# Kernel tuning notes

Hardware: AMD Instinct MI355X
Metric: run time of the kernel (lower is better)

The kernel has to match this reference:

```python
import jax, jax.numpy as jnp
import numpy as np

B, H, W = 16, 64, 64
C_IN, C_OUT, W_DIM = 256, 128, 128


def modulated_conv2d(x, kernel, style):
    """StyleGAN2 modulated+demodulated conv, vmapped over batch.
    x: [B,H,W,C_in], kernel: [kH,kW,C_in,C_out], style: [B,C_in]."""
    kH = kernel.shape[0]
    pad = kH // 2

    def conv_single(x_i, s_i):
        kern = kernel * s_i[None, None, :, None]
        denom = jnp.sqrt(jnp.sum(kern ** 2, axis=(0, 1, 2), keepdims=True) + 1e-08)
        kern = kern / denom
        return jax.lax.conv_general_dilated(
            x_i[None], kern, window_strides=(1, 1),
            padding=((pad, pad), (pad, pad)),
            dimension_numbers=('NHWC', 'HWIO', 'NHWC'))[0]

    return jax.vmap(conv_single)(x, style)


def pixel_shuffle(x, scale=2):
    b, h, w, c = x.shape
    s = scale
    c_out = c // (s * s)
    x = x.reshape(b, h, w, s, s, c_out)
    x = x.transpose(0, 1, 3, 2, 4, 5)
    return x.reshape(b, h * s, w * s, c_out)


def setup_inputs() -> dict:
    key = jax.random.key(0)
    ks = jax.random.split(key, 12)
    dense_std = 1.0 / np.sqrt(W_DIM)  # lecun_normal-like for Dense
    return {
        'x': jax.random.normal(ks[0], (B, H, W, C_IN), jnp.float32),
        'w': jax.random.normal(ks[1], (B, W_DIM), jnp.float32),
        'affine1_w': jax.random.normal(ks[2], (W_DIM, C_IN), jnp.float32) * dense_std,
        'affine1_b': jnp.ones((C_IN,), jnp.float32),  # bias_init=ones
        'kernel1': jax.random.normal(ks[3], (3, 3, C_IN, C_IN), jnp.float32),
        'noise_scale1': jnp.full((1,), 0.1, jnp.float32),
        'bias1': jax.random.normal(ks[4], (C_IN,), jnp.float32) * 0.02,
        'affine2_w': jax.random.normal(ks[5], (W_DIM, C_IN), jnp.float32) * dense_std,
        'affine2_b': jnp.ones((C_IN,), jnp.float32),
        'kernel2': jax.random.normal(ks[6], (3, 3, C_IN, C_OUT * 4), jnp.float32),
        'noise_scale2': jnp.full((1,), 0.1, jnp.float32),
        'bias2': jax.random.normal(ks[7], (C_OUT * 4,), jnp.float32) * 0.02,
        'noise1': jax.random.normal(ks[8], (B, H, W, 1), jnp.float32),
        'noise2': jax.random.normal(ks[9], (B, H, W, 1), jnp.float32),
    }


def reference(x, w, affine1_w, affine1_b, kernel1, noise_scale1, bias1,
              affine2_w, affine2_b, kernel2, noise_scale2, bias2,
              noise1, noise2):
    # style affine 1 -> modulated conv (C_in -> C_in)
    s1 = w @ affine1_w + affine1_b                      # [B, C_in]
    h = modulated_conv2d(x, kernel1, s1)                # [B,H,W,C_in]
    h = h + noise1 * noise_scale1
    h = jax.nn.leaky_relu(h + bias1, negative_slope=0.2)
    # style affine 2 -> modulated conv (C_in -> 4*C_out)
    s2 = w @ affine2_w + affine2_b                      # [B, C_in]
    h = modulated_conv2d(h, kernel2, s2)                # [B,H,W,4*C_out]
    h = h + noise2 * noise_scale2
    h = jax.nn.leaky_relu(h + bias2, negative_slope=0.2)
    return pixel_shuffle(h, scale=2)                    # [B,2H,2W,C_out]
```

## Files before the change

kernel.cpp:

```cpp
#include <hip/hip_runtime.h>
#include <type_traits>


#define CIN 256

typedef _Float16 half4 __attribute__((ext_vector_type(4)));
typedef _Float16 half8 __attribute__((ext_vector_type(8)));
typedef float f32x4 __attribute__((ext_vector_type(4)));

__global__ __launch_bounds__(256) void style_kernel(
    const float* __restrict__ w, const float* __restrict__ a1w, const float* __restrict__ a1b,
    const float* __restrict__ a2w, const float* __restrict__ a2b,
    float* __restrict__ s1, float* __restrict__ s2)
{
  const int b = blockIdx.x, c = threadIdx.x;
  const float* wb = w + b * 128;
  float acc1 = 0.f, acc2 = 0.f;
  for (int k = 0; k < 128; ++k) {
    const float wv = wb[k];
    acc1 = fmaf(wv, a1w[k * 256 + c], acc1);
    acc2 = fmaf(wv, a2w[k * 256 + c], acc2);
  }
  s1[b * 256 + c] = acc1 + a1b[c];
  s2[b * 256 + c] = acc2 + a2b[c];
}

__global__ __launch_bounds__(256) void ksq_kernel(
    const float* __restrict__ kern, float* __restrict__ ksq, int n)
{
  const int i = blockIdx.x * 256 + threadIdx.x;
  if (i < n) {
    float acc = 0.f;
    for (int t = 0; t < 9; ++t) { const float v = kern[t * n + i]; acc = fmaf(v, v, acc); }
    ksq[i] = acc;
  }
}

__global__ __launch_bounds__(256) void demod_kernel(
    const float* __restrict__ s, const float* __restrict__ ksq,
    float* __restrict__ demod, int cout)
{
  const int b = blockIdx.y;
  const int o = blockIdx.x * 256 + threadIdx.x;
  const float* sb = s + b * 256;
  float acc = 1e-8f;
  for (int i = 0; i < 256; ++i) {
    const float sv = sb[i];
    acc = fmaf(sv * sv, ksq[i * cout + o], acc);
  }
  demod[b * cout + o] = 1.0f / sqrtf(acc);
}

__global__ __launch_bounds__(256) void kprep_kernel(
    const float* __restrict__ Kw, _Float16* __restrict__ Bt, int cout)
{
  __shared__ float T[64][68];
  const int tap = blockIdx.z;
  const int o0 = blockIdx.x * 64, c0 = blockIdx.y * 64;
  const int t = threadIdx.x;
  #pragma unroll
  for (int it = 0; it < 4; ++it) {
    const int c = (t >> 4) + it * 16;
    const int o = (t & 15) * 4;
    *(float4*)(&T[c][o]) = *(const float4*)(Kw + ((size_t)tap * CIN + c0 + c) * cout + o0 + o);
  }
  __syncthreads();
  #pragma unroll
  for (int it = 0; it < 4; ++it) {
    const int o = (t >> 4) + it * 16;
    const int c = (t & 15) * 4;
    half4 hv = {(_Float16)T[c][o], (_Float16)T[c + 1][o],
                (_Float16)T[c + 2][o], (_Float16)T[c + 3][o]};
    *(half4*)(&Bt[((size_t)tap * cout + o0 + o) * CIN + c0 + c]) = hv;
  }
}

template <int COUT, bool SHUFFLE, typename TIN, typename TOUT>
__global__ __launch_bounds__(256) void conv_mfma(
    const TIN* __restrict__ X,
    const float* __restrict__ S,
    const _Float16* __restrict__ Bt,
    const float* __restrict__ D,
    const float* __restrict__ NZ,
    const float* __restrict__ NSp,
    const float* __restrict__ BIAS,
    TOUT* __restrict__ OUT)
{
  __shared__ __align__(16) _Float16 As[66][72];
  __shared__ __align__(16) _Float16 Bs[3][64][72];
  __shared__ float Ss[256];

  const int t = threadIdx.x;
  const int row = blockIdx.x;
  const int b = row >> 6, y = row & 63;
  const int o0 = blockIdx.y * 64;

  Ss[t] = S[b * 256 + t];

  const int lane = t & 63, wid = t >> 6;
  const int wm = wid >> 1, wn = wid & 1;
  const int lrow = lane >> 4;
  const int lcol = lane & 15;

  f32x4 acc[2][2];
  #pragma unroll
  for (int m = 0; m < 2; ++m)
    #pragma unroll
    for (int n = 0; n < 2; ++n)
      acc[m][n] = (f32x4){0.f, 0.f, 0.f, 0.f};

  const TIN* Xb = X + (size_t)b * (64 * 64 * CIN);

  for (int dyi = 0; dyi < 3; ++dyi) {
    const int ys = y + dyi - 1;
    const bool vrow = ((unsigned)ys < 64u);
    const TIN* Xrow = Xb + (size_t)ys * (64 * CIN);

    for (int c0 = 0; c0 < CIN; c0 += 64) {
      __syncthreads();
      #pragma unroll
      for (int it = 0; it < 5; ++it) {
        const int r = (t >> 4) + it * 16;
        if (r < 66) {
          const int xs = r - 1;
          const int cq = (t & 15) * 4;
          half4 hv = {(_Float16)0, (_Float16)0, (_Float16)0, (_Float16)0};
          if (vrow && (unsigned)xs < 64u) {
            const float4 sv = *(const float4*)(Ss + c0 + cq);
            if constexpr (std::is_same_v<TIN, float>) {
              const float4 xv = *(const float4*)(Xrow + (size_t)xs * CIN + c0 + cq);
              hv[0] = (_Float16)(xv.x * sv.x);
              hv[1] = (_Float16)(xv.y * sv.y);
              hv[2] = (_Float16)(xv.z * sv.z);
              hv[3] = (_Float16)(xv.w * sv.w);
            } else {
              const half4 xv = *(const half4*)(Xrow + (size_t)xs * CIN + c0 + cq);
              hv[0] = (_Float16)((float)xv[0] * sv.x);
              hv[1] = (_Float16)((float)xv[1] * sv.y);
              hv[2] = (_Float16)((float)xv[2] * sv.z);
              hv[3] = (_Float16)((float)xv[3] * sv.w);
            }
          }
          *(half4*)(&As[r][cq]) = hv;
        }
      }
      #pragma unroll
      for (int dxi = 0; dxi < 3; ++dxi) {
        const int tap = dyi * 3 + dxi;
        const _Float16* Bsrc = Bt + ((size_t)tap * COUT + o0) * CIN + c0;
        #pragma unroll
        for (int it = 0; it < 2; ++it) {
          const int n = (t >> 3) + it * 32;
          const int hq = (t & 7) * 8;
          *(half8*)(&Bs[dxi][n][hq]) = *(const half8*)(Bsrc + (size_t)n * CIN + hq);
        }
      }
      __syncthreads();
      #pragma unroll
      for (int dxi = 0; dxi < 3; ++dxi) {
        const int abase = dxi + wm * 32 + lcol;
        #pragma unroll
        for (int ks = 0; ks < 2; ++ks) {
          const int ko = ks * 32 + lrow * 8;
          const half8 a0 = *(const half8*)(&As[abase][ko]);
          const half8 a1 = *(const half8*)(&As[abase + 16][ko]);
          const half8 b0 = *(const half8*)(&Bs[dxi][wn * 32 + lcol][ko]);
          const half8 b1 = *(const half8*)(&Bs[dxi][wn * 32 + 16 + lcol][ko]);
          acc[0][0] = __builtin_amdgcn_mfma_f32_16x16x32_f16(a0, b0, acc[0][0], 0, 0, 0);
          acc[0][1] = __builtin_amdgcn_mfma_f32_16x16x32_f16(a0, b1, acc[0][1], 0, 0, 0);
          acc[1][0] = __builtin_amdgcn_mfma_f32_16x16x32_f16(a1, b0, acc[1][0], 0, 0, 0);
          acc[1][1] = __builtin_amdgcn_mfma_f32_16x16x32_f16(a1, b1, acc[1][1], 0, 0, 0);
        }
      }
    }
  }

  const float ns = NSp[0];
  #pragma unroll
  for (int n = 0; n < 2; ++n) {
    const int o = o0 + wn * 32 + n * 16 + lcol;
    const float dmv = D[b * COUT + o];
    const float bv = BIAS[o];
    #pragma unroll
    for (int m = 0; m < 2; ++m) {
      #pragma unroll
      for (int r = 0; r < 4; ++r) {
        const int p = wm * 32 + m * 16 + lrow * 4 + r;
        const float nzv = NZ[(size_t)(b * 64 + y) * 64 + p] * ns;
        float v = fmaf(acc[m][n][r], dmv, nzv + bv);
        v = fmaxf(v, 0.2f * v);
        if (!SHUFFLE) {
          OUT[((size_t)(b * 64 + y) * 64 + p) * COUT + o] = (TOUT)v;
        } else {
          const int g = o >> 7, c = o & 127;
          const int sh = g >> 1, sw = g & 1;
          OUT[(((size_t)(b * 128) + 2 * y + sh) * 128 + (2 * p + sw)) * 128 + c] = (TOUT)v;
        }
      }
    }
  }
}

extern "C" void kernel_launch(void* const* d_in, const int* in_sizes, int n_in,
                              void* d_out, int out_size, void* d_ws, size_t ws_size,
                              hipStream_t stream)
{
  const float* x   = (const float*)d_in[0];
  const float* w   = (const float*)d_in[1];
  const float* a1w = (const float*)d_in[2];
  const float* a1b = (const float*)d_in[3];
  const float* k1  = (const float*)d_in[4];
  const float* ns1 = (const float*)d_in[5];
  const float* b1  = (const float*)d_in[6];
  const float* a2w = (const float*)d_in[7];
  const float* a2b = (const float*)d_in[8];
  const float* k2  = (const float*)d_in[9];
  const float* ns2 = (const float*)d_in[10];
  const float* b2  = (const float*)d_in[11];
  const float* nz1 = (const float*)d_in[12];
  const float* nz2 = (const float*)d_in[13];
  float* out = (float*)d_out;

  float* ws = (float*)d_ws;
  float* s1   = ws;
  float* s2   = ws + 4096;
  float* ksq1 = ws + 8192;
  float* ksq2 = ws + 73728;
  float* dm1  = ws + 204800;
  float* dm2  = ws + 208896;
  _Float16* Bt1 = (_Float16*)(ws + 217088);
  _Float16* Bt2 = Bt1 + 9 * 256 * 256;
  _Float16* h   = Bt2 + 9 * 512 * 256;

  style_kernel<<<16, 256, 0, stream>>>(w, a1w, a1b, a2w, a2b, s1, s2);
  ksq_kernel<<<65536 / 256, 256, 0, stream>>>(k1, ksq1, 65536);
  ksq_kernel<<<131072 / 256, 256, 0, stream>>>(k2, ksq2, 131072);
  demod_kernel<<<dim3(1, 16), 256, 0, stream>>>(s1, ksq1, dm1, 256);
  demod_kernel<<<dim3(2, 16), 256, 0, stream>>>(s2, ksq2, dm2, 512);
  kprep_kernel<<<dim3(4, 4, 9), 256, 0, stream>>>(k1, Bt1, 256);
  kprep_kernel<<<dim3(8, 4, 9), 256, 0, stream>>>(k2, Bt2, 512);

  conv_mfma<256, false, float, _Float16><<<dim3(1024, 4), 256, 0, stream>>>(
      x, s1, Bt1, dm1, nz1, ns1, b1, h);
  conv_mfma<512, true, _Float16, float><<<dim3(1024, 8), 256, 0, stream>>>(
      h, s2, Bt2, dm2, nz2, ns2, b2, out);
}
```

Measured before the change: 696.9 us.

## Widen conv tiles to 128 outputs, fold style2 into conv1 epilogue, swizzle blocks

Each workgroup now computes 128 output channels with 512 threads, so every staged input row is reused across twice as many outputs. The second conv's style modulation is folded into the first conv's epilogue, letting conv2 load fp16 activations directly with no per-element multiply. A linear block index is remapped so that consecutive blocks are spread across groups of eight, which is meant to improve cache locality. In exchange the B tile in LDS doubles in size, which raises shared-memory use and may reduce occupancy.

```diff
diff --git a/kernel.cpp b/kernel.cpp
--- a/kernel.cpp
+++ b/kernel.cpp
@@ -75,32 +75,37 @@
   }
 }
 
-template <int COUT, bool SHUFFLE, typename TIN, typename TOUT>
-__global__ __launch_bounds__(256) void conv_mfma(
+template <int COUT, bool AMOD, bool SHUFFLE, typename TIN, typename TOUT>
+__global__ __launch_bounds__(512) void conv_mfma(
     const TIN* __restrict__ X,
-    const float* __restrict__ S,
+    const float* __restrict__ Sg,
     const _Float16* __restrict__ Bt,
     const float* __restrict__ D,
     const float* __restrict__ NZ,
     const float* __restrict__ NSp,
     const float* __restrict__ BIAS,
+    const float* __restrict__ SMOD,
     TOUT* __restrict__ OUT)
 {
   __shared__ __align__(16) _Float16 As[66][72];
-  __shared__ __align__(16) _Float16 Bs[3][64][72];
-  __shared__ float Ss[256];
+  __shared__ __align__(16) _Float16 Bs[3][128][72];
 
   const int t = threadIdx.x;
-  const int row = blockIdx.x;
+  constexpr int nwg = (COUT / 128) * 1024;
+  constexpr int q = nwg >> 3;
+  const int lin = blockIdx.x;
+  const int wgid = (lin & 7) * q + (lin >> 3);
+  const int row = wgid & 1023, oc = wgid >> 10;
   const int b = row >> 6, y = row & 63;
-  const int o0 = blockIdx.y * 64;
-
-  Ss[t] = S[b * 256 + t];
+  const int o0 = oc * 128;
 
   const int lane = t & 63, wid = t >> 6;
-  const int wm = wid >> 1, wn = wid & 1;
+  const int wm = wid & 1, wn = wid >> 1;
   const int lrow = lane >> 4;
   const int lcol = lane & 15;
+
+  const int sr = t >> 3;
+  const int sco = (t & 7) * 8;
 
   f32x4 acc[2][2];
   #pragma unroll
@@ -109,50 +114,48 @@
     for (int n = 0; n < 2; ++n)
       acc[m][n] = (f32x4){0.f, 0.f, 0.f, 0.f};
 
-  const TIN* Xb = X + (size_t)b * (64 * 64 * CIN);
+  const TIN* Xb = X + (size_t)b * (64 * 64 * 256);
 
   for (int dyi = 0; dyi < 3; ++dyi) {
     const int ys = y + dyi - 1;
     const bool vrow = ((unsigned)ys < 64u);
-    const TIN* Xrow = Xb + (size_t)ys * (64 * CIN);
-
-    for (int c0 = 0; c0 < CIN; c0 += 64) {
+    const TIN* Xrow = Xb + (size_t)(vrow ? ys : 0) * (64 * 256);
+
+    for (int c0 = 0; c0 < 256; c0 += 64) {
       __syncthreads();
       #pragma unroll
-      for (int it = 0; it < 5; ++it) {
-        const int r = (t >> 4) + it * 16;
-        if (r < 66) {
+      for (int part = 0; part < 2; ++part) {
+        const int r = part ? 64 + (t >> 3) : sr;
+        if (part == 0 || t < 16) {
           const int xs = r - 1;
-          const int cq = (t & 15) * 4;
-          half4 hv = {(_Float16)0, (_Float16)0, (_Float16)0, (_Float16)0};
-          if (vrow && (unsigned)xs < 64u) {
-            const float4 sv = *(const float4*)(Ss + c0 + cq);
-            if constexpr (std::is_same_v<TIN, float>) {
-              const float4 xv = *(const float4*)(Xrow + (size_t)xs * CIN + c0 + cq);
-              hv[0] = (_Float16)(xv.x * sv.x);
-              hv[1] = (_Float16)(xv.y * sv.y);
-              hv[2] = (_Float16)(xv.z * sv.z);
-              hv[3] = (_Float16)(xv.w * sv.w);
+          const bool v = vrow && ((unsigned)xs < 64u);
+          half8 hv = {(_Float16)0, (_Float16)0, (_Float16)0, (_Float16)0,
+                      (_Float16)0, (_Float16)0, (_Float16)0, (_Float16)0};
+          if (v) {
+            if constexpr (AMOD) {
+              const float4 x0 = *(const float4*)(Xrow + (size_t)xs * 256 + c0 + sco);
+              const float4 x1 = *(const float4*)(Xrow + (size_t)xs * 256 + c0 + sco + 4);
+              const float4 s0 = *(const float4*)(Sg + b * 256 + c0 + sco);
+              const float4 s1v = *(const float4*)(Sg + b * 256 + c0 + sco + 4);
+              hv[0] = (_Float16)(x0.x * s0.x);  hv[1] = (_Float16)(x0.y * s0.y);
+              hv[2] = (_Float16)(x0.z * s0.z);  hv[3] = (_Float16)(x0.w * s0.w);
+              hv[4] = (_Float16)(x1.x * s1v.x); hv[5] = (_Float16)(x1.y * s1v.y);
+              hv[6] = (_Float16)(x1.z * s1v.z); hv[7] = (_Float16)(x1.w * s1v.w);
             } else {
-              const half4 xv = *(const half4*)(Xrow + (size_t)xs * CIN + c0 + cq);
-              hv[0] = (_Float16)((float)xv[0] * sv.x);
-              hv[1] = (_Float16)((float)xv[1] * sv.y);
-              hv[2] = (_Float16)((float)xv[2] * sv.z);
-              hv[3] = (_Float16)((float)xv[3] * sv.w);
+              hv = *(const half8*)(Xrow + (size_t)xs * 256 + c0 + sco);
             }
           }
-          *(half4*)(&As[r][cq]) = hv;
+          *(half8*)(&As[r][sco]) = hv;
         }
       }
       #pragma unroll
       for (int dxi = 0; dxi < 3; ++dxi) {
         const int tap = dyi * 3 + dxi;
-        const _Float16* Bsrc = Bt + ((size_t)tap * COUT + o0) * CIN + c0;
+        const _Float16* Bsrc = Bt + ((size_t)tap * COUT + o0) * 256 + c0;
         #pragma unroll
-        for (int it = 0; it < 2; ++it) {
-          const int n = (t >> 3) + it * 32;
-          const int hq = (t & 7) * 8;
-          *(half8*)(&Bs[dxi][n][hq]) = *(const half8*)(Bsrc + (size_t)n * CIN + hq);
+        for (int pass = 0; pass < 2; ++pass) {
+          const int n = (t >> 3) + pass * 64;
+          *(half8*)(&Bs[dxi][n][sco]) = *(const half8*)(Bsrc + (size_t)n * 256 + sco);
         }
       }
       __syncthreads();
@@ -181,6 +184,8 @@
     const int o = o0 + wn * 32 + n * 16 + lcol;
     const float dmv = D[b * COUT + o];
     const float bv = BIAS[o];
+    float smv = 1.0f;
+    if constexpr (!SHUFFLE) smv = SMOD[b * 256 + o];
     #pragma unroll
     for (int m = 0; m < 2; ++m) {
       #pragma unroll
@@ -189,8 +194,8 @@
         const float nzv = NZ[(size_t)(b * 64 + y) * 64 + p] * ns;
         float v = fmaf(acc[m][n][r], dmv, nzv + bv);
         v = fmaxf(v, 0.2f * v);
-        if (!SHUFFLE) {
-          OUT[((size_t)(b * 64 + y) * 64 + p) * COUT + o] = (TOUT)v;
+        if constexpr (!SHUFFLE) {
+          OUT[((size_t)(b * 64 + y) * 64 + p) * COUT + o] = (TOUT)(v * smv);
         } else {
           const int g = o >> 7, c = o & 127;
           const int sh = g >> 1, sw = g & 1;
@@ -230,7 +235,7 @@
   float* dm2  = ws + 208896;
   _Float16* Bt1 = (_Float16*)(ws + 217088);
   _Float16* Bt2 = Bt1 + 9 * 256 * 256;
-  _Float16* h   = Bt2 + 9 * 512 * 256;
+  _Float16* h2m = Bt2 + 9 * 512 * 256;
 
   style_kernel<<<16, 256, 0, stream>>>(w, a1w, a1b, a2w, a2b, s1, s2);
   ksq_kernel<<<65536 / 256, 256, 0, stream>>>(k1, ksq1, 65536);
@@ -240,8 +245,8 @@
   kprep_kernel<<<dim3(4, 4, 9), 256, 0, stream>>>(k1, Bt1, 256);
   kprep_kernel<<<dim3(8, 4, 9), 256, 0, stream>>>(k2, Bt2, 512);
 
-  conv_mfma<256, false, float, _Float16><<<dim3(1024, 4), 256, 0, stream>>>(
-      x, s1, Bt1, dm1, nz1, ns1, b1, h);
-  conv_mfma<512, true, _Float16, float><<<dim3(1024, 8), 256, 0, stream>>>(
-      h, s2, Bt2, dm2, nz2, ns2, b2, out);
-}
+  conv_mfma<256, true, false, float, _Float16><<<2048, 512, 0, stream>>>(
+      x, s1, Bt1, dm1, nz1, ns1, b1, s2, h2m);
+  conv_mfma<512, false, true, _Float16, float><<<4096, 512, 0, stream>>>(
+      h2m, nullptr, Bt2, dm2, nz2, ns2, b2, nullptr, out);
+}
```

Result: faster. 582.1 us (-16.5%).
